# Kernel optimization log

Measured on AMD Instinct MI355X. Metric: run time of the kernel, lower is better.

Reference implementation:

```python
import jax, jax.numpy as jnp
import numpy as np

NUM_GROUPS = 32
EPS = 1e-6


def group_norm(x, gamma, beta):
    # x: [B, C, H, W]
    B, C, H, W = x.shape
    xg = x.reshape(B, NUM_GROUPS, C // NUM_GROUPS, H, W)
    mean = jnp.mean(xg, axis=(2, 3, 4), keepdims=True)
    var = jnp.var(xg, axis=(2, 3, 4), keepdims=True)
    xn = ((xg - mean) * jax.lax.rsqrt(var + EPS)).reshape(B, C, H, W)
    return xn * gamma[None, :, None, None] + beta[None, :, None, None]


def conv1x1(x, w, b):
    # x: [B, C, H, W], w: [O, C], b: [O]  (1x1 conv == channel matmul)
    return jnp.einsum('oc,bchw->bohw', w, x) + b[None, :, None, None]


def setup_inputs() -> dict:
    key = jax.random.key(0)
    ks = jax.random.split(key, 10)
    B, C, H, W = 16, 512, 32, 32
    s = 1.0 / np.sqrt(C)
    inp = {
        'hidden_states': jax.random.normal(ks[0], (B, C, H, W), dtype=jnp.float32),
        'norm_gamma': jnp.ones((C,), dtype=jnp.float32),
        'norm_beta': jnp.zeros((C,), dtype=jnp.float32),
        'wq': jax.random.normal(ks[1], (C, C), dtype=jnp.float32) * s,
        'bq': jnp.zeros((C,), dtype=jnp.float32),
        'wk': jax.random.normal(ks[2], (C, C), dtype=jnp.float32) * s,
        'bk': jnp.zeros((C,), dtype=jnp.float32),
        'wv': jax.random.normal(ks[3], (C, C), dtype=jnp.float32) * s,
        'bv': jnp.zeros((C,), dtype=jnp.float32),
        'wo': jax.random.normal(ks[4], (C, C), dtype=jnp.float32) * s,
        'bo': jnp.zeros((C,), dtype=jnp.float32),
    }
    return inp


def reference(hidden_states, norm_gamma, norm_beta, wq, bq, wk, bk, wv, bv, wo, bo):
    residual = hidden_states
    h = group_norm(hidden_states, norm_gamma, norm_beta)
    q = conv1x1(h, wq, bq)  # [B, C, H, W]
    k = conv1x1(h, wk, bk)
    v = conv1x1(h, wv, bv)
    B, C, H, W = q.shape
    N = H * W
    qf = q.reshape(B, C, N)  # [B, C, N]
    kf = k.reshape(B, C, N)
    vf = v.reshape(B, C, N)
    scale = float(C) ** (-0.5)
    # attn_weights[b, i, j] = sum_c q[b,c,i] * k[b,c,j]
    attn = jnp.einsum('bci,bcj->bij', qf, kf) * scale
    attn = jax.nn.softmax(attn, axis=2)
    # out[b, c, i] = sum_j v[b,c,j] * attn[b,i,j]
    out = jnp.einsum('bcj,bij->bci', vf, attn).reshape(B, C, H, W)
    out = conv1x1(out, wo, bo)
    return residual + out
```

## Files before the change

kernel.cpp:

```cpp
#include <hip/hip_runtime.h>

typedef __attribute__((ext_vector_type(4))) float f32x4;
typedef __attribute__((ext_vector_type(8))) __bf16 bf16x8;
typedef __attribute__((ext_vector_type(4))) unsigned short us4;
typedef __attribute__((ext_vector_type(8))) unsigned short us8;

#define B_  16
#define C_  512
#define N_  1024
#define G_  32
#define GS  16

__device__ inline unsigned short f2bf(float f) {
  unsigned u = __builtin_bit_cast(unsigned, f);
  u += 0x7fffu + ((u >> 16) & 1u);
  return (unsigned short)(u >> 16);
}

#define GLOAD_LDS16(gp, lp) __builtin_amdgcn_global_load_lds( \
    (const __attribute__((address_space(1))) unsigned int*)(gp), \
    (__attribute__((address_space(3))) unsigned int*)(lp), 16, 0, 0)

__global__ __launch_bounds__(256) void gn_stats(const float* __restrict__ x,
                                                float* __restrict__ stats) {
  int bg = blockIdx.x;
  const float* xp = x + (long)bg * (GS * N_);
  int tid = threadIdx.x;
  float s = 0.f, ss = 0.f;
  for (int i = tid * 4; i < GS * N_; i += 1024) {
    f32x4 v = *(const f32x4*)&xp[i];
    s += v.x + v.y + v.z + v.w;
    ss += v.x * v.x + v.y * v.y + v.z * v.z + v.w * v.w;
  }
  __shared__ float r1[256], r2[256];
  r1[tid] = s; r2[tid] = ss; __syncthreads();
  for (int off = 128; off > 0; off >>= 1) {
    if (tid < off) { r1[tid] += r1[tid + off]; r2[tid] += r2[tid + off]; }
    __syncthreads();
  }
  if (tid == 0) {
    float mean = r1[0] * (1.f / (GS * N_));
    float var  = r2[0] * (1.f / (GS * N_)) - mean * mean;
    stats[bg * 2]     = mean;
    stats[bg * 2 + 1] = rsqrtf(var + 1e-6f);
  }
}

__global__ __launch_bounds__(256) void gn_apply(const float* __restrict__ x,
                                                const float* __restrict__ stats,
                                                const float* __restrict__ gamma,
                                                const float* __restrict__ beta,
                                                unsigned short* __restrict__ ht) {
  int b = blockIdx.z, ct = blockIdx.y, nt = blockIdx.x;
  int c0 = ct * 64, n0 = nt * 64;
  int tid = threadIdx.x;
  __shared__ unsigned short L[64 * 68];
  const float* xp = x + ((long)b * C_ + c0) * N_ + n0;
#pragma unroll
  for (int i = 0; i < 4; ++i) {
    int li = tid + i * 256;
    int row = li >> 4;
    int col4 = (li & 15) * 4;
    f32x4 v = *(const f32x4*)&xp[(long)row * N_ + col4];
    int c = c0 + row;
    float mean = stats[(b * G_ + (c >> 4)) * 2];
    float rstd = stats[(b * G_ + (c >> 4)) * 2 + 1];
    float gm = gamma[c] * rstd;
    float bt = beta[c] - mean * gm;
    us4 o;
    o.x = f2bf(v.x * gm + bt); o.y = f2bf(v.y * gm + bt);
    o.z = f2bf(v.z * gm + bt); o.w = f2bf(v.w * gm + bt);
    *(us4*)&L[row * 68 + col4] = o;
  }
  __syncthreads();
#pragma unroll
  for (int i = 0; i < 2; ++i) {
    int s = tid + i * 256;
    int n = s >> 3;
    int cs = (s & 7) * 8;
    us8 o;
#pragma unroll
    for (int j = 0; j < 8; ++j) o[j] = L[(cs + j) * 68 + n];
    *(us8*)&ht[((long)b * N_ + n0 + n) * C_ + c0 + cs] = o;
  }
}

__global__ __launch_bounds__(256) void convert_w(const float* __restrict__ wq, const float* __restrict__ wk,
                                                 const float* __restrict__ wo,
                                                 const float* __restrict__ bq, const float* __restrict__ bk,
                                                 const float* __restrict__ bv,
                                                 unsigned short* __restrict__ wqk,
                                                 unsigned short* __restrict__ wob, float* __restrict__ bqk,
                                                 float* __restrict__ bvo) {
  long bid = blockIdx.x;
  int tid = threadIdx.x;
  long i = bid * 256 + tid;
  if (i < C_ * C_) {
    wqk[i]           = f2bf(wq[i]);
    wqk[C_ * C_ + i] = f2bf(wk[i]);
    wob[i]           = f2bf(wo[i]);
  }
  if (i < C_) { bqk[i] = bq[i]; bqk[C_ + i] = bk[i]; }
  if (bid >= 1024) {
    int o = (int)(bid - 1024) * 256 + tid;
    const float* wr = wo + (long)o * 512;
    float acc = 0.f;
    for (int c = 0; c < 512; c += 4) {
      f32x4 w4 = *(const f32x4*)&wr[c];
      f32x4 b4 = *(const f32x4*)&bv[c];
      acc += w4.x * b4.x + w4.y * b4.y + w4.z * b4.z + w4.w * b4.w;
    }
    bvo[o] = acc;
  }
}

__global__ __launch_bounds__(256) void transpose_wv(const float* __restrict__ wv,
                                                    unsigned short* __restrict__ wvT) {
  int c0 = blockIdx.x * 64, k0 = blockIdx.y * 64;
  int tid = threadIdx.x;
  __shared__ float Lt[64][65];
#pragma unroll
  for (int i = 0; i < 4; ++i) {
    int lin = tid + i * 256;
    int rr = lin >> 4;
    int q4 = (lin & 15) * 4;
    f32x4 v = *(const f32x4*)&wv[(long)(c0 + rr) * 512 + k0 + q4];
    Lt[q4 + 0][rr] = v.x; Lt[q4 + 1][rr] = v.y;
    Lt[q4 + 2][rr] = v.z; Lt[q4 + 3][rr] = v.w;
  }
  __syncthreads();
#pragma unroll
  for (int i = 0; i < 2; ++i) {
    int lin = tid + i * 256;
    int kk = lin >> 3;
    int cc = (lin & 7) * 8;
    us8 o;
#pragma unroll
    for (int j = 0; j < 8; ++j) o[j] = f2bf(Lt[kk][cc + j]);
    *(us8*)&wvT[(long)(k0 + kk) * 512 + c0 + cc] = o;
  }
}

__device__ inline f32x4 mfma16(bf16x8 a, bf16x8 b, f32x4 c) {
  return __builtin_amdgcn_mfma_f32_16x16x32_bf16(a, b, c, 0, 0, 0);
}

__global__ __launch_bounds__(256) void wprod(const unsigned short* __restrict__ wob,
                                             const unsigned short* __restrict__ wvT,
                                             unsigned short* __restrict__ WVO) {
  int row0 = blockIdx.x * 64, col0 = blockIdx.y * 64;
  int tid = threadIdx.x, lane = tid & 63, w = tid >> 6;
  int lr = lane & 15, kh = (lane >> 4) * 8;
  f32x4 acc4[4];
#pragma unroll
  for (int n = 0; n < 4; ++n) acc4[n] = f32x4{0.f, 0.f, 0.f, 0.f};
  for (int k0 = 0; k0 < 512; k0 += 32) {
    bf16x8 af = *(const bf16x8*)&wob[(long)(row0 + w * 16 + lr) * 512 + k0 + kh];
#pragma unroll
    for (int n = 0; n < 4; ++n) {
      bf16x8 bf8 = *(const bf16x8*)&wvT[(long)(col0 + n * 16 + lr) * 512 + k0 + kh];
      acc4[n] = mfma16(af, bf8, acc4[n]);
    }
  }
  int rb = (lane >> 4) * 4;
#pragma unroll
  for (int n = 0; n < 4; ++n)
#pragma unroll
    for (int r = 0; r < 4; ++r)
      WVO[(long)(row0 + w * 16 + rb + r) * 512 + col0 + n * 16 + lr] = f2bf(acc4[n][r]);
}

__device__ inline int swz(int b) { return b ^ (((b >> 9) & 1) << 5); }

template<int EPI, int SHX, int SHY, int XSWZ>
__global__ __launch_bounds__(256, 2) void gemm128(
    const unsigned short* __restrict__ A, long lda, long Az,
    const unsigned short* __restrict__ Bm, long ldb, long Bz,
    void* __restrict__ Dp, long ldd, long Dz,
    const float* __restrict__ bias, float scale, int K,
    const float* __restrict__ residual, float* __restrict__ rs) {
  int bx = blockIdx.x, by = blockIdx.y, bz = blockIdx.z;
  if constexpr (XSWZ) {
    int lin = bx + ((by + (bz << SHY)) << SHX);
    int cpx = 1 << (SHX + SHY + 4 - 3);
    int l2  = (lin & 7) * cpx + (lin >> 3);
    bx = l2 & ((1 << SHX) - 1);
    by = (l2 >> SHX) & ((1 << SHY) - 1);
    bz = l2 >> (SHX + SHY);
  }
  const int z = bz;
  const long row0 = (long)bx * 128;
  const long col0 = (long)by * 128;
  const int tid  = threadIdx.x;
  const int lane = tid & 63;
  const int wave = tid >> 6;
  const int wm = wave >> 1;
  const int wn = wave & 1;
  const int lr = lane & 15;
  const int khb = (lane >> 4) * 16;

  __shared__ unsigned short Abuf[2][8192];
  __shared__ unsigned short Bbuf[2][8192];
  __shared__ float sred[128];

  const unsigned short* Ab = A  + (long)z * Az;
  const unsigned short* Bb = Bm + (long)z * Bz;

  if constexpr (EPI == 7) {
    if (tid < 128) {
      const float* rp = rs + ((long)z * 1024 + row0 + tid) * 16;
      float s = 0.f;
#pragma unroll
      for (int i = 0; i < 16; ++i) s += rp[i];
      sred[tid] = 1.f / s;
    }
    asm volatile("s_waitcnt lgkmcnt(0)" ::: "memory");
  }

  const unsigned short* gA[4];
  const unsigned short* gB[4];
#pragma unroll
  for (int r = 0; r < 4; ++r) {
    int L = swz(r * 4096 + tid * 16);
    gA[r] = Ab + (row0 + (L >> 7)) * lda + ((L & 127) >> 1);
    gB[r] = Bb + (col0 + (L >> 7)) * ldb + ((L & 127) >> 1);
  }

  f32x4 acc[4][4];
#pragma unroll
  for (int m = 0; m < 4; ++m)
#pragma unroll
    for (int n = 0; n < 4; ++n) acc[m][n] = f32x4{0.f, 0.f, 0.f, 0.f};

  const int NT = K >> 6;
  const int ldsO = wave * 512;

#pragma unroll
  for (int r = 0; r < 4; ++r) {
    GLOAD_LDS16(gA[r], &Abuf[0][r * 2048 + ldsO]);
    GLOAD_LDS16(gB[r], &Bbuf[0][r * 2048 + ldsO]);
  }

  for (int t = 0; t < NT; ++t) {
    int tn = t + 1; if (tn == NT) tn = 0;
    const long ko = (long)tn << 6;
    const int nb = (t + 1) & 1;
#pragma unroll
    for (int r = 0; r < 4; ++r) {
      GLOAD_LDS16(gA[r] + ko, &Abuf[nb][r * 2048 + ldsO]);
      GLOAD_LDS16(gB[r] + ko, &Bbuf[nb][r * 2048 + ldsO]);
    }
    asm volatile("s_waitcnt vmcnt(8)" ::: "memory");
    __builtin_amdgcn_s_barrier();
    __builtin_amdgcn_sched_barrier(0);
    const unsigned short* Al = Abuf[t & 1];
    const unsigned short* Bl = Bbuf[t & 1];
#pragma unroll
    for (int kk = 0; kk < 2; ++kk) {
      bf16x8 af[4], bfr[4];
#pragma unroll
      for (int m = 0; m < 4; ++m) {
        int Pb = swz((wm * 64 + m * 16 + lr) * 128 + kk * 64 + khb);
        af[m] = *(const bf16x8*)((const char*)Al + Pb);
      }
#pragma unroll
      for (int n = 0; n < 4; ++n) {
        int Pb = swz((wn * 64 + n * 16 + lr) * 128 + kk * 64 + khb);
        bfr[n] = *(const bf16x8*)((const char*)Bl + Pb);
      }
      __builtin_amdgcn_s_setprio(1);
#pragma unroll
      for (int m = 0; m < 4; ++m)
#pragma unroll
        for (int n = 0; n < 4; ++n)
          acc[m][n] = mfma16(af[m], bfr[n], acc[m][n]);
      __builtin_amdgcn_s_setprio(0);
    }
    __builtin_amdgcn_sched_barrier(0);
    __builtin_amdgcn_s_barrier();
    __builtin_amdgcn_sched_barrier(0);
  }
  asm volatile("s_waitcnt vmcnt(0)" ::: "memory");
  __builtin_amdgcn_s_barrier();

  const int rb = (lane >> 4) * 4;

  if constexpr (EPI == 7) {
#pragma unroll
    for (int m = 0; m < 4; ++m) {
      int lrow = wm * 64 + m * 16 + rb;
      long gr0 = row0 + lrow;
#pragma unroll
      for (int n = 0; n < 4; ++n) {
        long gc = col0 + wn * 64 + n * 16 + lr;
        long o = (long)z * (512L * 1024L) + gc * 1024L + gr0;
        f32x4 res = *(const f32x4*)&residual[o];
        float bb = bias[gc];
        f32x4 st;
#pragma unroll
        for (int r = 0; r < 4; ++r)
          st[r] = acc[m][n][r] * sred[lrow + r] + bb + res[r];
        *(f32x4*)&((float*)Dp)[o] = st;
      }
    }
    return;
  }

  float* slab = ((float*)(void*)Abuf) + wave * 1088;
  const int jt = by;
  unsigned short* Dst = (unsigned short*)Dp + (long)z * Dz;
#pragma unroll
  for (int m = 0; m < 4; ++m) {
    float ps[4] = {0.f, 0.f, 0.f, 0.f};
#pragma unroll
    for (int n = 0; n < 4; ++n) {
      float bcol = 0.f;
      if constexpr (EPI == 0) bcol = bias[col0 + wn * 64 + n * 16 + lr];
#pragma unroll
      for (int r = 0; r < 4; ++r) {
        float v = acc[m][n][r];
        if constexpr (EPI == 0) v += bcol;
        else if constexpr (EPI == 1) v += bias[row0 + wm * 64 + m * 16 + rb + r];
        else if constexpr (EPI == 5) { v = exp2f(v * scale); ps[r] += v; }
        slab[(rb + r) * 68 + n * 16 + lr] = v;
      }
    }
    if constexpr (EPI == 5) {
#pragma unroll
      for (int r = 0; r < 4; ++r) {
        ps[r] += __shfl_xor(ps[r], 1);
        ps[r] += __shfl_xor(ps[r], 2);
        ps[r] += __shfl_xor(ps[r], 4);
        ps[r] += __shfl_xor(ps[r], 8);
      }
      if (lr == 0) {
#pragma unroll
        for (int r = 0; r < 4; ++r)
          rs[((long)z * 1024 + row0 + wm * 64 + m * 16 + rb + r) * 16 + jt * 2 + wn] = ps[r];
      }
    }
#pragma unroll
    for (int p = 0; p < 2; ++p) {
      int rl = p * 8 + (lane >> 3);
      int c8 = (lane & 7) * 8;
      f32x4 v0 = *(const f32x4*)&slab[rl * 68 + c8];
      f32x4 v1 = *(const f32x4*)&slab[rl * 68 + c8 + 4];
      us8 o;
      o[0] = f2bf(v0.x); o[1] = f2bf(v0.y); o[2] = f2bf(v0.z); o[3] = f2bf(v0.w);
      o[4] = f2bf(v1.x); o[5] = f2bf(v1.y); o[6] = f2bf(v1.z); o[7] = f2bf(v1.w);
      *(us8*)&Dst[(row0 + wm * 64 + m * 16 + rl) * ldd + col0 + wn * 64 + c8] = o;
    }
  }
}

extern "C" void kernel_launch(void* const* d_in, const int* in_sizes, int n_in,
                              void* d_out, int out_size, void* d_ws, size_t ws_size,
                              hipStream_t stream) {
  const float* x     = (const float*)d_in[0];
  const float* gamma = (const float*)d_in[1];
  const float* beta  = (const float*)d_in[2];
  const float* wq    = (const float*)d_in[3];
  const float* bq    = (const float*)d_in[4];
  const float* wk    = (const float*)d_in[5];
  const float* bk    = (const float*)d_in[6];
  const float* wv    = (const float*)d_in[7];
  const float* bv    = (const float*)d_in[8];
  const float* wo    = (const float*)d_in[9];
  const float* bo    = (const float*)d_in[10];
  float* out = (float*)d_out;

  char* ws = (char*)d_ws;
  unsigned short* ht   = (unsigned short*)(ws + 0);
  unsigned short* qkt  = (unsigned short*)(ws + 16777216);
  unsigned short* VWT  = (unsigned short*)(ws + 50331648);
  unsigned short* S    = (unsigned short*)(ws + 83886080);
  unsigned short* wqkb = (unsigned short*)(ws + 117440512);
  unsigned short* wvT  = (unsigned short*)(ws + 119537664);
  unsigned short* wob  = (unsigned short*)(ws + 120061952);
  unsigned short* WVO  = (unsigned short*)(ws + 120586240);
  float* bqk           = (float*)(ws + 121110528);
  float* bvo           = (float*)(ws + 121114624);
  float* stats         = (float*)(ws + 121116672);
  float* rs            = (float*)(ws + 121122816);

  convert_w<<<1026, 256, 0, stream>>>(wq, wk, wo, bq, bk, bv,
                                      wqkb, wob, bqk, bvo);
  transpose_wv<<<dim3(8, 8), 256, 0, stream>>>(wv, wvT);
  wprod<<<dim3(8, 8), 256, 0, stream>>>(wob, wvT, WVO);
  gn_stats<<<512, 256, 0, stream>>>(x, stats);
  gn_apply<<<dim3(16, 8, 16), 256, 0, stream>>>(x, stats, gamma, beta, ht);

  gemm128<0, 0, 0, 0><<<dim3(128, 8, 1), 256, 0, stream>>>(ht, 512, 0, wqkb, 512, 0,
                                                           qkt, 1024, 0, bqk, 0.f, 512, nullptr, nullptr);
  gemm128<1, 0, 0, 0><<<dim3(4, 128, 1), 256, 0, stream>>>(WVO, 512, 0, ht, 512, 0,
                                                           VWT, 16384, 0, bvo, 0.f, 512, nullptr, nullptr);
  gemm128<5, 3, 3, 1><<<dim3(8, 8, 16), 256, 0, stream>>>(qkt, 1024, 1048576L, qkt + 512, 1024, 1048576L,
                                                          S, 1024, 1048576L, nullptr,
                                                          0.06375871416f, 512, nullptr, rs);
  gemm128<7, 3, 2, 1><<<dim3(8, 4, 16), 256, 0, stream>>>(S, 1024, 1048576L,
                                                          VWT, 16384, 1024,
                                                          out, 0, 0, bo, 0.f, 1024, x, rs);
}
```

Baseline: 152.5 us.

## Fuse QK^T softmax and PV into a single attention kernel per query tile

```diff
diff --git a/kernel.cpp b/kernel.cpp
--- a/kernel.cpp
+++ b/kernel.cpp
@@ -172,25 +172,14 @@
 
 __device__ inline int swz(int b) { return b ^ (((b >> 9) & 1) << 5); }
 
-template<int EPI, int SHX, int SHY, int XSWZ>
+template<int EPI>
 __global__ __launch_bounds__(256, 2) void gemm128(
-    const unsigned short* __restrict__ A, long lda, long Az,
-    const unsigned short* __restrict__ Bm, long ldb, long Bz,
-    void* __restrict__ Dp, long ldd, long Dz,
-    const float* __restrict__ bias, float scale, int K,
-    const float* __restrict__ residual, float* __restrict__ rs) {
-  int bx = blockIdx.x, by = blockIdx.y, bz = blockIdx.z;
-  if constexpr (XSWZ) {
-    int lin = bx + ((by + (bz << SHY)) << SHX);
-    int cpx = 1 << (SHX + SHY + 4 - 3);
-    int l2  = (lin & 7) * cpx + (lin >> 3);
-    bx = l2 & ((1 << SHX) - 1);
-    by = (l2 >> SHX) & ((1 << SHY) - 1);
-    bz = l2 >> (SHX + SHY);
-  }
-  const int z = bz;
-  const long row0 = (long)bx * 128;
-  const long col0 = (long)by * 128;
+    const unsigned short* __restrict__ A, long lda,
+    const unsigned short* __restrict__ Bm, long ldb,
+    void* __restrict__ Dp, long ldd,
+    const float* __restrict__ bias, int K) {
+  const long row0 = (long)blockIdx.x * 128;
+  const long col0 = (long)blockIdx.y * 128;
   const int tid  = threadIdx.x;
   const int lane = tid & 63;
   const int wave = tid >> 6;
@@ -201,29 +190,14 @@
 
   __shared__ unsigned short Abuf[2][8192];
   __shared__ unsigned short Bbuf[2][8192];
-  __shared__ float sred[128];
-
-  const unsigned short* Ab = A  + (long)z * Az;
-  const unsigned short* Bb = Bm + (long)z * Bz;
-
-  if constexpr (EPI == 7) {
-    if (tid < 128) {
-      const float* rp = rs + ((long)z * 1024 + row0 + tid) * 16;
-      float s = 0.f;
-#pragma unroll
-      for (int i = 0; i < 16; ++i) s += rp[i];
-      sred[tid] = 1.f / s;
-    }
-    asm volatile("s_waitcnt lgkmcnt(0)" ::: "memory");
-  }
 
   const unsigned short* gA[4];
   const unsigned short* gB[4];
 #pragma unroll
   for (int r = 0; r < 4; ++r) {
     int L = swz(r * 4096 + tid * 16);
-    gA[r] = Ab + (row0 + (L >> 7)) * lda + ((L & 127) >> 1);
-    gB[r] = Bb + (col0 + (L >> 7)) * ldb + ((L & 127) >> 1);
+    gA[r] = A  + (row0 + (L >> 7)) * lda + ((L & 127) >> 1);
+    gB[r] = Bm + (col0 + (L >> 7)) * ldb + ((L & 127) >> 1);
   }
 
   f32x4 acc[4][4];
@@ -284,34 +258,10 @@
   __builtin_amdgcn_s_barrier();
 
   const int rb = (lane >> 4) * 4;
-
-  if constexpr (EPI == 7) {
-#pragma unroll
-    for (int m = 0; m < 4; ++m) {
-      int lrow = wm * 64 + m * 16 + rb;
-      long gr0 = row0 + lrow;
-#pragma unroll
-      for (int n = 0; n < 4; ++n) {
-        long gc = col0 + wn * 64 + n * 16 + lr;
-        long o = (long)z * (512L * 1024L) + gc * 1024L + gr0;
-        f32x4 res = *(const f32x4*)&residual[o];
-        float bb = bias[gc];
-        f32x4 st;
-#pragma unroll
-        for (int r = 0; r < 4; ++r)
-          st[r] = acc[m][n][r] * sred[lrow + r] + bb + res[r];
-        *(f32x4*)&((float*)Dp)[o] = st;
-      }
-    }
-    return;
-  }
-
   float* slab = ((float*)(void*)Abuf) + wave * 1088;
-  const int jt = by;
-  unsigned short* Dst = (unsigned short*)Dp + (long)z * Dz;
+  unsigned short* Dst = (unsigned short*)Dp;
 #pragma unroll
   for (int m = 0; m < 4; ++m) {
-    float ps[4] = {0.f, 0.f, 0.f, 0.f};
 #pragma unroll
     for (int n = 0; n < 4; ++n) {
       float bcol = 0.f;
@@ -320,23 +270,8 @@
       for (int r = 0; r < 4; ++r) {
         float v = acc[m][n][r];
         if constexpr (EPI == 0) v += bcol;
-        else if constexpr (EPI == 1) v += bias[row0 + wm * 64 + m * 16 + rb + r];
-        else if constexpr (EPI == 5) { v = exp2f(v * scale); ps[r] += v; }
+        else                    v += bias[row0 + wm * 64 + m * 16 + rb + r];
         slab[(rb + r) * 68 + n * 16 + lr] = v;
-      }
-    }
-    if constexpr (EPI == 5) {
-#pragma unroll
-      for (int r = 0; r < 4; ++r) {
-        ps[r] += __shfl_xor(ps[r], 1);
-        ps[r] += __shfl_xor(ps[r], 2);
-        ps[r] += __shfl_xor(ps[r], 4);
-        ps[r] += __shfl_xor(ps[r], 8);
-      }
-      if (lr == 0) {
-#pragma unroll
-        for (int r = 0; r < 4; ++r)
-          rs[((long)z * 1024 + row0 + wm * 64 + m * 16 + rb + r) * 16 + jt * 2 + wn] = ps[r];
       }
     }
 #pragma unroll
@@ -349,6 +284,125 @@
       o[0] = f2bf(v0.x); o[1] = f2bf(v0.y); o[2] = f2bf(v0.z); o[3] = f2bf(v0.w);
       o[4] = f2bf(v1.x); o[5] = f2bf(v1.y); o[6] = f2bf(v1.z); o[7] = f2bf(v1.w);
       *(us8*)&Dst[(row0 + wm * 64 + m * 16 + rl) * ldd + col0 + wn * 64 + c8] = o;
+    }
+  }
+}
+
+__global__ __launch_bounds__(256, 2) void fa_kernel(const unsigned short* __restrict__ qkt,
+                                                    const unsigned short* __restrict__ VWT,
+                                                    const float* __restrict__ bo,
+                                                    const float* __restrict__ x,
+                                                    float* __restrict__ out) {
+  int lin = blockIdx.x;
+  int l2  = (lin & 7) * 64 + (lin >> 3);
+  int qt = l2 & 31, z = l2 >> 5;
+  const int tid  = threadIdx.x;
+  const int lane = tid & 63;
+  const int wave = tid >> 6;
+  const int lr = lane & 15;
+  const int kh = (lane >> 4) * 8;
+  const int rb = (lane >> 4) * 4;
+
+  __shared__ unsigned short Sp[32][1032];
+  __shared__ float rsP[4][32];
+  __shared__ float dinv[32];
+
+  const unsigned short* Qb = qkt + ((long)z * 1024 + qt * 32) * 1024;
+  const unsigned short* Kb = qkt + (long)z * 1024 * 1024 + 512;
+
+  const float scale = 0.06375871416f;
+  float psum[2][4];
+#pragma unroll
+  for (int m = 0; m < 2; ++m)
+#pragma unroll
+    for (int r = 0; r < 4; ++r) psum[m][r] = 0.f;
+
+  for (int jt = 0; jt < 8; ++jt) {
+    f32x4 acc[2][2];
+#pragma unroll
+    for (int m = 0; m < 2; ++m)
+#pragma unroll
+      for (int n = 0; n < 2; ++n) acc[m][n] = f32x4{0.f, 0.f, 0.f, 0.f};
+    for (int kc = 0; kc < 16; ++kc) {
+      bf16x8 aq[2], bk_[2];
+#pragma unroll
+      for (int m = 0; m < 2; ++m)
+        aq[m] = *(const bf16x8*)&Qb[(long)(m * 16 + lr) * 1024 + kc * 32 + kh];
+#pragma unroll
+      for (int n = 0; n < 2; ++n)
+        bk_[n] = *(const bf16x8*)&Kb[(long)(jt * 128 + wave * 32 + n * 16 + lr) * 1024 + kc * 32 + kh];
+#pragma unroll
+      for (int m = 0; m < 2; ++m)
+#pragma unroll
+        for (int n = 0; n < 2; ++n)
+          acc[m][n] = mfma16(aq[m], bk_[n], acc[m][n]);
+    }
+#pragma unroll
+    for (int m = 0; m < 2; ++m)
+#pragma unroll
+      for (int n = 0; n < 2; ++n)
+#pragma unroll
+        for (int r = 0; r < 4; ++r) {
+          float e = exp2f(acc[m][n][r] * scale);
+          psum[m][r] += e;
+          Sp[m * 16 + rb + r][jt * 128 + wave * 32 + n * 16 + lr] = f2bf(e);
+        }
+  }
+#pragma unroll
+  for (int m = 0; m < 2; ++m)
+#pragma unroll
+    for (int r = 0; r < 4; ++r) {
+      psum[m][r] += __shfl_xor(psum[m][r], 1);
+      psum[m][r] += __shfl_xor(psum[m][r], 2);
+      psum[m][r] += __shfl_xor(psum[m][r], 4);
+      psum[m][r] += __shfl_xor(psum[m][r], 8);
+    }
+  if (lr == 0) {
+#pragma unroll
+    for (int m = 0; m < 2; ++m)
+#pragma unroll
+      for (int r = 0; r < 4; ++r)
+        rsP[wave][m * 16 + rb + r] = psum[m][r];
+  }
+  __syncthreads();
+  if (tid < 32) dinv[tid] = 1.f / (rsP[0][tid] + rsP[1][tid] + rsP[2][tid] + rsP[3][tid]);
+  __syncthreads();
+
+  const unsigned short* Vb = VWT + (long)z * 1024;
+  for (int ot = 0; ot < 4; ++ot) {
+    f32x4 acc2[2][2];
+#pragma unroll
+    for (int m = 0; m < 2; ++m)
+#pragma unroll
+      for (int n = 0; n < 2; ++n) acc2[m][n] = f32x4{0.f, 0.f, 0.f, 0.f};
+    for (int jc = 0; jc < 32; ++jc) {
+      bf16x8 ap[2], bv_[2];
+#pragma unroll
+      for (int m = 0; m < 2; ++m)
+        ap[m] = *(const bf16x8*)&Sp[m * 16 + lr][jc * 32 + kh];
+#pragma unroll
+      for (int n = 0; n < 2; ++n)
+        bv_[n] = *(const bf16x8*)&Vb[(long)(ot * 128 + wave * 32 + n * 16 + lr) * 16384 + jc * 32 + kh];
+#pragma unroll
+      for (int m = 0; m < 2; ++m)
+#pragma unroll
+        for (int n = 0; n < 2; ++n)
+          acc2[m][n] = mfma16(ap[m], bv_[n], acc2[m][n]);
+    }
+#pragma unroll
+    for (int m = 0; m < 2; ++m) {
+#pragma unroll
+      for (int n = 0; n < 2; ++n) {
+        int o = ot * 128 + wave * 32 + n * 16 + lr;
+        long ad = ((long)z * 512 + o) * 1024 + qt * 32 + m * 16 + rb;
+        f32x4 res = *(const f32x4*)&x[ad];
+        float bb = bo[o];
+        f32x4 st;
+#pragma unroll
+        for (int r = 0; r < 4; ++r)
+          st[r] = acc2[m][n][r] * dinv[m * 16 + rb + r] + bb + res[r];
+        *(f32x4*)&out[ad] = st;
+      }
     }
   }
 }
@@ -373,7 +427,6 @@
   unsigned short* ht   = (unsigned short*)(ws + 0);
   unsigned short* qkt  = (unsigned short*)(ws + 16777216);
   unsigned short* VWT  = (unsigned short*)(ws + 50331648);
-  unsigned short* S    = (unsigned short*)(ws + 83886080);
   unsigned short* wqkb = (unsigned short*)(ws + 117440512);
   unsigned short* wvT  = (unsigned short*)(ws + 119537664);
   unsigned short* wob  = (unsigned short*)(ws + 120061952);
@@ -381,7 +434,6 @@
   float* bqk           = (float*)(ws + 121110528);
   float* bvo           = (float*)(ws + 121114624);
   float* stats         = (float*)(ws + 121116672);
-  float* rs            = (float*)(ws + 121122816);
 
   convert_w<<<1026, 256, 0, stream>>>(wq, wk, wo, bq, bk, bv,
                                       wqkb, wob, bqk, bvo);
@@ -390,14 +442,7 @@
   gn_stats<<<512, 256, 0, stream>>>(x, stats);
   gn_apply<<<dim3(16, 8, 16), 256, 0, stream>>>(x, stats, gamma, beta, ht);
 
-  gemm128<0, 0, 0, 0><<<dim3(128, 8, 1), 256, 0, stream>>>(ht, 512, 0, wqkb, 512, 0,
-                                                           qkt, 1024, 0, bqk, 0.f, 512, nullptr, nullptr);
-  gemm128<1, 0, 0, 0><<<dim3(4, 128, 1), 256, 0, stream>>>(WVO, 512, 0, ht, 512, 0,
-                                                           VWT, 16384, 0, bvo, 0.f, 512, nullptr, nullptr);
-  gemm128<5, 3, 3, 1><<<dim3(8, 8, 16), 256, 0, stream>>>(qkt, 1024, 1048576L, qkt + 512, 1024, 1048576L,
-                                                          S, 1024, 1048576L, nullptr,
-                                                          0.06375871416f, 512, nullptr, rs);
-  gemm128<7, 3, 2, 1><<<dim3(8, 4, 16), 256, 0, stream>>>(S, 1024, 1048576L,
-                                                          VWT, 16384, 1024,
-                                                          out, 0, 0, bo, 0.f, 1024, x, rs);
-}
+  gemm128<0><<<dim3(128, 8), 256, 0, stream>>>(ht, 512, wqkb, 512, qkt, 1024, bqk, 512);
+  gemm128<1><<<dim3(4, 128), 256, 0, stream>>>(WVO, 512, ht, 512, VWT, 16384, bvo, 512);
+  fa_kernel<<<512, 256, 0, stream>>>(qkt, VWT, bo, x, out);
+}
```

After: 217.4 us. 42.5% more time.

## Fuse group-norm stats and apply, merge QK and VWO projection GEMMs into one launch

Applied to the files above, without the earlier changes.

```diff
diff --git a/kernel.cpp b/kernel.cpp
--- a/kernel.cpp
+++ b/kernel.cpp
@@ -21,67 +21,49 @@
     (const __attribute__((address_space(1))) unsigned int*)(gp), \
     (__attribute__((address_space(3))) unsigned int*)(lp), 16, 0, 0)
 
-__global__ __launch_bounds__(256) void gn_stats(const float* __restrict__ x,
-                                                float* __restrict__ stats) {
+__global__ __launch_bounds__(256) void gn_fused(const float* __restrict__ x,
+                                                const float* __restrict__ gamma,
+                                                const float* __restrict__ beta,
+                                                unsigned short* __restrict__ ht) {
   int bg = blockIdx.x;
-  const float* xp = x + (long)bg * (GS * N_);
+  int b = bg >> 5, g = bg & 31;
   int tid = threadIdx.x;
+  __shared__ float Lx[16][1028];
+  __shared__ float r1[256], r2[256];
+  const float* xp = x + ((long)b * C_ + g * 16) * N_;
   float s = 0.f, ss = 0.f;
-  for (int i = tid * 4; i < GS * N_; i += 1024) {
-    f32x4 v = *(const f32x4*)&xp[i];
-    s += v.x + v.y + v.z + v.w;
+#pragma unroll
+  for (int i = 0; i < 16; ++i) {
+    f32x4 v = *(const f32x4*)&xp[(long)i * N_ + tid * 4];
+    s  += v.x + v.y + v.z + v.w;
     ss += v.x * v.x + v.y * v.y + v.z * v.z + v.w * v.w;
-  }
-  __shared__ float r1[256], r2[256];
+    *(f32x4*)&Lx[i][tid * 4] = v;
+  }
   r1[tid] = s; r2[tid] = ss; __syncthreads();
   for (int off = 128; off > 0; off >>= 1) {
     if (tid < off) { r1[tid] += r1[tid + off]; r2[tid] += r2[tid + off]; }
     __syncthreads();
   }
-  if (tid == 0) {
-    float mean = r1[0] * (1.f / (GS * N_));
-    float var  = r2[0] * (1.f / (GS * N_)) - mean * mean;
-    stats[bg * 2]     = mean;
-    stats[bg * 2 + 1] = rsqrtf(var + 1e-6f);
-  }
-}
-
-__global__ __launch_bounds__(256) void gn_apply(const float* __restrict__ x,
-                                                const float* __restrict__ stats,
-                                                const float* __restrict__ gamma,
-                                                const float* __restrict__ beta,
-                                                unsigned short* __restrict__ ht) {
-  int b = blockIdx.z, ct = blockIdx.y, nt = blockIdx.x;
-  int c0 = ct * 64, n0 = nt * 64;
-  int tid = threadIdx.x;
-  __shared__ unsigned short L[64 * 68];
-  const float* xp = x + ((long)b * C_ + c0) * N_ + n0;
-#pragma unroll
-  for (int i = 0; i < 4; ++i) {
-    int li = tid + i * 256;
-    int row = li >> 4;
-    int col4 = (li & 15) * 4;
-    f32x4 v = *(const f32x4*)&xp[(long)row * N_ + col4];
-    int c = c0 + row;
-    float mean = stats[(b * G_ + (c >> 4)) * 2];
-    float rstd = stats[(b * G_ + (c >> 4)) * 2 + 1];
-    float gm = gamma[c] * rstd;
-    float bt = beta[c] - mean * gm;
-    us4 o;
-    o.x = f2bf(v.x * gm + bt); o.y = f2bf(v.y * gm + bt);
-    o.z = f2bf(v.z * gm + bt); o.w = f2bf(v.w * gm + bt);
-    *(us4*)&L[row * 68 + col4] = o;
-  }
-  __syncthreads();
-#pragma unroll
-  for (int i = 0; i < 2; ++i) {
-    int s = tid + i * 256;
-    int n = s >> 3;
-    int cs = (s & 7) * 8;
+  float mean = r1[0] * (1.f / 16384.f);
+  float var  = r2[0] * (1.f / 16384.f) - mean * mean;
+  float rstd = rsqrtf(var + 1e-6f);
+  float gm[8], bt[8];
+  int cbase = g * 16 + (tid & 1) * 8;
+#pragma unroll
+  for (int k = 0; k < 8; ++k) {
+    gm[k] = gamma[cbase + k] * rstd;
+    bt[k] = beta[cbase + k] - mean * gm[k];
+  }
+#pragma unroll
+  for (int j = 0; j < 8; ++j) {
+    int lin = tid + j * 256;
+    int n = lin >> 1;
+    int c8 = (lin & 1) * 8;
     us8 o;
 #pragma unroll
-    for (int j = 0; j < 8; ++j) o[j] = L[(cs + j) * 68 + n];
-    *(us8*)&ht[((long)b * N_ + n0 + n) * C_ + c0 + cs] = o;
+    for (int k = 0; k < 8; ++k)
+      o[k] = f2bf(Lx[c8 + k][n] * gm[k] + bt[k]);
+    *(us8*)&ht[((long)b * N_ + n) * C_ + g * 16 + c8] = o;
   }
 }
 
@@ -171,6 +153,130 @@
 }
 
 __device__ inline int swz(int b) { return b ^ (((b >> 9) & 1) << 5); }
+
+__global__ __launch_bounds__(256, 2) void gemm12(
+    const unsigned short* __restrict__ ht, const unsigned short* __restrict__ wqkb,
+    const unsigned short* __restrict__ WVO,
+    unsigned short* __restrict__ qkt, unsigned short* __restrict__ VWT,
+    const float* __restrict__ bqk, const float* __restrict__ bvo) {
+  const int bid = blockIdx.x;
+  const int sel = ((bid % 3) == 2);
+  const unsigned short* A;  const unsigned short* Bm;
+  unsigned short* Dst; const float* bias;
+  long lda, ldb, ldd, row0, col0;
+  if (!sel) {
+    int g1 = (bid / 3) * 2 + (bid % 3);
+    row0 = (long)(g1 & 127) * 128; col0 = (long)(g1 >> 7) * 128;
+    A = ht;  lda = 512; Bm = wqkb; ldb = 512; Dst = qkt; ldd = 1024; bias = bqk;
+  } else {
+    int g2 = bid / 3;
+    row0 = (long)(g2 & 3) * 128; col0 = (long)(g2 >> 2) * 128;
+    A = WVO; lda = 512; Bm = ht;  ldb = 512; Dst = VWT; ldd = 16384; bias = bvo;
+  }
+  const int tid  = threadIdx.x;
+  const int lane = tid & 63;
+  const int wave = tid >> 6;
+  const int wm = wave >> 1;
+  const int wn = wave & 1;
+  const int lr = lane & 15;
+  const int khb = (lane >> 4) * 16;
+
+  __shared__ unsigned short Abuf[2][8192];
+  __shared__ unsigned short Bbuf[2][8192];
+
+  const unsigned short* gA[4];
+  const unsigned short* gB[4];
+#pragma unroll
+  for (int r = 0; r < 4; ++r) {
+    int L = swz(r * 4096 + tid * 16);
+    gA[r] = A  + (row0 + (L >> 7)) * lda + ((L & 127) >> 1);
+    gB[r] = Bm + (col0 + (L >> 7)) * ldb + ((L & 127) >> 1);
+  }
+
+  f32x4 acc[4][4];
+#pragma unroll
+  for (int m = 0; m < 4; ++m)
+#pragma unroll
+    for (int n = 0; n < 4; ++n) acc[m][n] = f32x4{0.f, 0.f, 0.f, 0.f};
+
+  const int NT = 8;
+  const int ldsO = wave * 512;
+
+#pragma unroll
+  for (int r = 0; r < 4; ++r) {
+    GLOAD_LDS16(gA[r], &Abuf[0][r * 2048 + ldsO]);
+    GLOAD_LDS16(gB[r], &Bbuf[0][r * 2048 + ldsO]);
+  }
+
+  for (int t = 0; t < NT; ++t) {
+    int tn = t + 1; if (tn == NT) tn = 0;
+    const long ko = (long)tn << 6;
+    const int nb = (t + 1) & 1;
+#pragma unroll
+    for (int r = 0; r < 4; ++r) {
+      GLOAD_LDS16(gA[r] + ko, &Abuf[nb][r * 2048 + ldsO]);
+      GLOAD_LDS16(gB[r] + ko, &Bbuf[nb][r * 2048 + ldsO]);
+    }
+    asm volatile("s_waitcnt vmcnt(8)" ::: "memory");
+    __builtin_amdgcn_s_barrier();
+    __builtin_amdgcn_sched_barrier(0);
+    const unsigned short* Al = Abuf[t & 1];
+    const unsigned short* Bl = Bbuf[t & 1];
+#pragma unroll
+    for (int kk = 0; kk < 2; ++kk) {
+      bf16x8 af[4], bfr[4];
+#pragma unroll
+      for (int m = 0; m < 4; ++m) {
+        int Pb = swz((wm * 64 + m * 16 + lr) * 128 + kk * 64 + khb);
+        af[m] = *(const bf16x8*)((const char*)Al + Pb);
+      }
+#pragma unroll
+      for (int n = 0; n < 4; ++n) {
+        int Pb = swz((wn * 64 + n * 16 + lr) * 128 + kk * 64 + khb);
+        bfr[n] = *(const bf16x8*)((const char*)Bl + Pb);
+      }
+      __builtin_amdgcn_s_setprio(1);
+#pragma unroll
+      for (int m = 0; m < 4; ++m)
+#pragma unroll
+        for (int n = 0; n < 4; ++n)
+          acc[m][n] = mfma16(af[m], bfr[n], acc[m][n]);
+      __builtin_amdgcn_s_setprio(0);
+    }
+    __builtin_amdgcn_sched_barrier(0);
+    __builtin_amdgcn_s_barrier();
+    __builtin_amdgcn_sched_barrier(0);
+  }
+  asm volatile("s_waitcnt vmcnt(0)" ::: "memory");
+  __builtin_amdgcn_s_barrier();
+
+  const int rb = (lane >> 4) * 4;
+  float* slab = ((float*)(void*)Abuf) + wave * 1088;
+#pragma unroll
+  for (int m = 0; m < 4; ++m) {
+#pragma unroll
+    for (int n = 0; n < 4; ++n) {
+      float bcol = sel ? 0.f : bias[col0 + wn * 64 + n * 16 + lr];
+#pragma unroll
+      for (int r = 0; r < 4; ++r) {
+        float v = acc[m][n][r];
+        v += sel ? bias[row0 + wm * 64 + m * 16 + rb + r] : bcol;
+        slab[(rb + r) * 68 + n * 16 + lr] = v;
+      }
+    }
+#pragma unroll
+    for (int p = 0; p < 2; ++p) {
+      int rl = p * 8 + (lane >> 3);
+      int c8 = (lane & 7) * 8;
+      f32x4 v0 = *(const f32x4*)&slab[rl * 68 + c8];
+      f32x4 v1 = *(const f32x4*)&slab[rl * 68 + c8 + 4];
+      us8 o;
+      o[0] = f2bf(v0.x); o[1] = f2bf(v0.y); o[2] = f2bf(v0.z); o[3] = f2bf(v0.w);
+      o[4] = f2bf(v1.x); o[5] = f2bf(v1.y); o[6] = f2bf(v1.z); o[7] = f2bf(v1.w);
+      *(us8*)&Dst[(row0 + wm * 64 + m * 16 + rl) * ldd + col0 + wn * 64 + c8] = o;
+    }
+  }
+}
 
 template<int EPI, int SHX, int SHY, int XSWZ>
 __global__ __launch_bounds__(256, 2) void gemm128(
@@ -314,30 +420,24 @@
     float ps[4] = {0.f, 0.f, 0.f, 0.f};
 #pragma unroll
     for (int n = 0; n < 4; ++n) {
-      float bcol = 0.f;
-      if constexpr (EPI == 0) bcol = bias[col0 + wn * 64 + n * 16 + lr];
 #pragma unroll
       for (int r = 0; r < 4; ++r) {
-        float v = acc[m][n][r];
-        if constexpr (EPI == 0) v += bcol;
-        else if constexpr (EPI == 1) v += bias[row0 + wm * 64 + m * 16 + rb + r];
-        else if constexpr (EPI == 5) { v = exp2f(v * scale); ps[r] += v; }
+        float v = exp2f(acc[m][n][r] * scale);
+        ps[r] += v;
         slab[(rb + r) * 68 + n * 16 + lr] = v;
       }
     }
-    if constexpr (EPI == 5) {
-#pragma unroll
-      for (int r = 0; r < 4; ++r) {
-        ps[r] += __shfl_xor(ps[r], 1);
-        ps[r] += __shfl_xor(ps[r], 2);
-        ps[r] += __shfl_xor(ps[r], 4);
-        ps[r] += __shfl_xor(ps[r], 8);
-      }
-      if (lr == 0) {
-#pragma unroll
-        for (int r = 0; r < 4; ++r)
-          rs[((long)z * 1024 + row0 + wm * 64 + m * 16 + rb + r) * 16 + jt * 2 + wn] = ps[r];
-      }
+#pragma unroll
+    for (int r = 0; r < 4; ++r) {
+      ps[r] += __shfl_xor(ps[r], 1);
+      ps[r] += __shfl_xor(ps[r], 2);
+      ps[r] += __shfl_xor(ps[r], 4);
+      ps[r] += __shfl_xor(ps[r], 8);
+    }
+    if (lr == 0) {
+#pragma unroll
+      for (int r = 0; r < 4; ++r)
+        rs[((long)z * 1024 + row0 + wm * 64 + m * 16 + rb + r) * 16 + jt * 2 + wn] = ps[r];
     }
 #pragma unroll
     for (int p = 0; p < 2; ++p) {
@@ -380,20 +480,15 @@
   unsigned short* WVO  = (unsigned short*)(ws + 120586240);
   float* bqk           = (float*)(ws + 121110528);
   float* bvo           = (float*)(ws + 121114624);
-  float* stats         = (float*)(ws + 121116672);
   float* rs            = (float*)(ws + 121122816);
 
   convert_w<<<1026, 256, 0, stream>>>(wq, wk, wo, bq, bk, bv,
                                       wqkb, wob, bqk, bvo);
   transpose_wv<<<dim3(8, 8), 256, 0, stream>>>(wv, wvT);
   wprod<<<dim3(8, 8), 256, 0, stream>>>(wob, wvT, WVO);
-  gn_stats<<<512, 256, 0, stream>>>(x, stats);
-  gn_apply<<<dim3(16, 8, 16), 256, 0, stream>>>(x, stats, gamma, beta, ht);
-
-  gemm128<0, 0, 0, 0><<<dim3(128, 8, 1), 256, 0, stream>>>(ht, 512, 0, wqkb, 512, 0,
-                                                           qkt, 1024, 0, bqk, 0.f, 512, nullptr, nullptr);
-  gemm128<1, 0, 0, 0><<<dim3(4, 128, 1), 256, 0, stream>>>(WVO, 512, 0, ht, 512, 0,
-                                                           VWT, 16384, 0, bvo, 0.f, 512, nullptr, nullptr);
+  gn_fused<<<512, 256, 0, stream>>>(x, gamma, beta, ht);
+
+  gemm12<<<1536, 256, 0, stream>>>(ht, wqkb, WVO, qkt, VWT, bqk, bvo);
   gemm128<5, 3, 3, 1><<<dim3(8, 8, 16), 256, 0, stream>>>(qkt, 1024, 1048576L, qkt + 512, 1024, 1048576L,
                                                           S, 1024, 1048576L, nullptr,
                                                           0.06375871416f, 512, nullptr, rs);
```

New measurement: 158.1 us. 3.6% more time.

## Fuse group-norm stats and apply into one kernel with the group cached in LDS

Applied to the files above, without the earlier changes.

```diff
diff --git a/kernel.cpp b/kernel.cpp
--- a/kernel.cpp
+++ b/kernel.cpp
@@ -21,67 +21,49 @@
     (const __attribute__((address_space(1))) unsigned int*)(gp), \
     (__attribute__((address_space(3))) unsigned int*)(lp), 16, 0, 0)
 
-__global__ __launch_bounds__(256) void gn_stats(const float* __restrict__ x,
-                                                float* __restrict__ stats) {
+__global__ __launch_bounds__(256) void gn_fused(const float* __restrict__ x,
+                                                const float* __restrict__ gamma,
+                                                const float* __restrict__ beta,
+                                                unsigned short* __restrict__ ht) {
   int bg = blockIdx.x;
-  const float* xp = x + (long)bg * (GS * N_);
+  int b = bg >> 5, g = bg & 31;
   int tid = threadIdx.x;
+  __shared__ float Lx[16][1028];
+  __shared__ float r1[256], r2[256];
+  const float* xp = x + ((long)b * C_ + g * 16) * N_;
   float s = 0.f, ss = 0.f;
-  for (int i = tid * 4; i < GS * N_; i += 1024) {
-    f32x4 v = *(const f32x4*)&xp[i];
-    s += v.x + v.y + v.z + v.w;
+#pragma unroll
+  for (int i = 0; i < 16; ++i) {
+    f32x4 v = *(const f32x4*)&xp[(long)i * N_ + tid * 4];
+    s  += v.x + v.y + v.z + v.w;
     ss += v.x * v.x + v.y * v.y + v.z * v.z + v.w * v.w;
-  }
-  __shared__ float r1[256], r2[256];
+    *(f32x4*)&Lx[i][tid * 4] = v;
+  }
   r1[tid] = s; r2[tid] = ss; __syncthreads();
   for (int off = 128; off > 0; off >>= 1) {
     if (tid < off) { r1[tid] += r1[tid + off]; r2[tid] += r2[tid + off]; }
     __syncthreads();
   }
-  if (tid == 0) {
-    float mean = r1[0] * (1.f / (GS * N_));
-    float var  = r2[0] * (1.f / (GS * N_)) - mean * mean;
-    stats[bg * 2]     = mean;
-    stats[bg * 2 + 1] = rsqrtf(var + 1e-6f);
-  }
-}
-
-__global__ __launch_bounds__(256) void gn_apply(const float* __restrict__ x,
-                                                const float* __restrict__ stats,
-                                                const float* __restrict__ gamma,
-                                                const float* __restrict__ beta,
-                                                unsigned short* __restrict__ ht) {
-  int b = blockIdx.z, ct = blockIdx.y, nt = blockIdx.x;
-  int c0 = ct * 64, n0 = nt * 64;
-  int tid = threadIdx.x;
-  __shared__ unsigned short L[64 * 68];
-  const float* xp = x + ((long)b * C_ + c0) * N_ + n0;
-#pragma unroll
-  for (int i = 0; i < 4; ++i) {
-    int li = tid + i * 256;
-    int row = li >> 4;
-    int col4 = (li & 15) * 4;
-    f32x4 v = *(const f32x4*)&xp[(long)row * N_ + col4];
-    int c = c0 + row;
-    float mean = stats[(b * G_ + (c >> 4)) * 2];
-    float rstd = stats[(b * G_ + (c >> 4)) * 2 + 1];
-    float gm = gamma[c] * rstd;
-    float bt = beta[c] - mean * gm;
-    us4 o;
-    o.x = f2bf(v.x * gm + bt); o.y = f2bf(v.y * gm + bt);
-    o.z = f2bf(v.z * gm + bt); o.w = f2bf(v.w * gm + bt);
-    *(us4*)&L[row * 68 + col4] = o;
-  }
-  __syncthreads();
-#pragma unroll
-  for (int i = 0; i < 2; ++i) {
-    int s = tid + i * 256;
-    int n = s >> 3;
-    int cs = (s & 7) * 8;
+  float mean = r1[0] * (1.f / 16384.f);
+  float var  = r2[0] * (1.f / 16384.f) - mean * mean;
+  float rstd = rsqrtf(var + 1e-6f);
+  float gm[8], bt[8];
+  int cbase = g * 16 + (tid & 1) * 8;
+#pragma unroll
+  for (int k = 0; k < 8; ++k) {
+    gm[k] = gamma[cbase + k] * rstd;
+    bt[k] = beta[cbase + k] - mean * gm[k];
+  }
+#pragma unroll
+  for (int j = 0; j < 8; ++j) {
+    int lin = tid + j * 256;
+    int n = lin >> 1;
+    int c8 = (lin & 1) * 8;
     us8 o;
 #pragma unroll
-    for (int j = 0; j < 8; ++j) o[j] = L[(cs + j) * 68 + n];
-    *(us8*)&ht[((long)b * N_ + n0 + n) * C_ + c0 + cs] = o;
+    for (int k = 0; k < 8; ++k)
+      o[k] = f2bf(Lx[c8 + k][n] * gm[k] + bt[k]);
+    *(us8*)&ht[((long)b * N_ + n) * C_ + g * 16 + c8] = o;
   }
 }
 
@@ -380,15 +362,13 @@
   unsigned short* WVO  = (unsigned short*)(ws + 120586240);
   float* bqk           = (float*)(ws + 121110528);
   float* bvo           = (float*)(ws + 121114624);
-  float* stats         = (float*)(ws + 121116672);
   float* rs            = (float*)(ws + 121122816);
 
   convert_w<<<1026, 256, 0, stream>>>(wq, wk, wo, bq, bk, bv,
                                       wqkb, wob, bqk, bvo);
   transpose_wv<<<dim3(8, 8), 256, 0, stream>>>(wv, wvT);
   wprod<<<dim3(8, 8), 256, 0, stream>>>(wob, wvT, WVO);
-  gn_stats<<<512, 256, 0, stream>>>(x, stats);
-  gn_apply<<<dim3(16, 8, 16), 256, 0, stream>>>(x, stats, gamma, beta, ht);
+  gn_fused<<<512, 256, 0, stream>>>(x, gamma, beta, ht);
 
   gemm128<0, 0, 0, 0><<<dim3(128, 8, 1), 256, 0, stream>>>(ht, 512, 0, wqkb, 512, 0,
                                                            qkt, 1024, 0, bqk, 0.f, 512, nullptr, nullptr);
```

After: 147.6 us. -3.3%, faster.
